# Optimization experiments

Hardware: AMD Instinct MI355X
Metric: run time of the kernel (lower is better)

## Reference

```python
import jax, jax.numpy as jnp
from jax import lax
import numpy as np

B, S, D, H, O, V = 1024, 128, 256, 2048, 10, 10

def setup_inputs() -> dict:
    key = jax.random.key(0)
    ks = jax.random.split(key, 8)
    x = jax.random.randint(ks[0], (B, S), 0, V)
    embed = jax.random.normal(ks[1], (V, D), dtype=jnp.float32)
    sd_hx = 1.0 / np.sqrt(D)
    sd_hh = 1.0 / np.sqrt(H)
    W_hx = jax.random.uniform(ks[2], (H, D), minval=-sd_hx, maxval=sd_hx)
    b_hx = jax.random.uniform(ks[3], (H,), minval=-sd_hx, maxval=sd_hx)
    W_hh = jax.random.uniform(ks[4], (H, H), minval=-sd_hh, maxval=sd_hh)
    b_hh = jax.random.uniform(ks[5], (H,), minval=-sd_hh, maxval=sd_hh)
    W_oh = jax.random.uniform(ks[6], (O, H), minval=-sd_hh, maxval=sd_hh)
    b_oh = jax.random.uniform(ks[7], (O,), minval=-sd_hh, maxval=sd_hh)
    return {"x": x, "embed": embed, "W_hx": W_hx, "b_hx": b_hx,
            "W_hh": W_hh, "b_hh": b_hh, "W_oh": W_oh, "b_oh": b_oh}

def reference(x, embed, W_hx, b_hx, W_hh, b_hh, W_oh, b_oh):
    e = embed[x]                                   # [B,S,D]
    # precompute input-to-hidden projection for all steps (one big GEMM)
    xh = jnp.einsum('bsd,hd->bsh', e, W_hx) + b_hx  # [B,S,H]
    # step 0: torch code applies ONLY hx (no hh term, no hh bias)
    h0 = jnp.tanh(xh[:, 0])
    def step(h, xt):
        h = jnp.tanh(xt + h @ W_hh.T + b_hh)
        return h, None
    hT, _ = lax.scan(step, h0, jnp.swapaxes(xh[:, 1:], 0, 1))  # scan over time
    o = hT @ W_oh.T + b_oh                         # [B,O]
    return jax.nn.softmax(o, axis=1)               # nn.Softmax() on 2D -> dim=1
```

## Files before the change

kernel.cpp:

```cpp
#include <hip/hip_runtime.h>
#include <stdint.h>
#include <stddef.h>

#define B_ 1024
#define S_ 128
#define D_ 256
#define H_ 2048
#define O_ 10
#define V_ 10

#define BM 128
#define BN 64
#define BK 128
#define NKT (H_ / BK)
#define NSTG 3
#define STG_ELEMS ((BM + BN) * BK)
#define SMEM_BYTES (NSTG * STG_ELEMS * 2)

typedef unsigned short u16;
typedef short v8s __attribute__((ext_vector_type(8)));
typedef float v4f __attribute__((ext_vector_type(4)));
typedef u16 u16x4 __attribute__((ext_vector_type(4)));

__device__ __forceinline__ u16 f2bf(float f) {
  unsigned int u = __float_as_uint(f);
  u += 0x7FFFu + ((u >> 16) & 1u);
  return (u16)(u >> 16);
}
__device__ __forceinline__ float bf2f(u16 h) {
  return __uint_as_float(((unsigned int)h) << 16);
}
__device__ __forceinline__ float fast_tanh(float x) {
  float e = __expf(2.0f * x);
  return 1.0f - 2.0f / (e + 1.0f);
}
__device__ __forceinline__ void gl2lds16(const void* g, void* l) {
  __builtin_amdgcn_global_load_lds(
      (const __attribute__((address_space(1))) uint32_t*)g,
      (__attribute__((address_space(3))) uint32_t*)l, 16, 0, 0);
}

__global__ __launch_bounds__(256) void make_table(const float* __restrict__ embed,
                                                  const float* __restrict__ W_hx,
                                                  const float* __restrict__ b_hx,
                                                  float* __restrict__ Txh) {
  int idx = blockIdx.x * 256 + threadIdx.x;
  int v = idx >> 11, h = idx & 2047;
  const float4* e4 = (const float4*)(embed + v * D_);
  const float4* w4 = (const float4*)(W_hx + (size_t)h * D_);
  float s = b_hx[h];
#pragma unroll 4
  for (int d = 0; d < D_ / 4; ++d) {
    float4 a = e4[d], b = w4[d];
    s = fmaf(a.x, b.x, s); s = fmaf(a.y, b.y, s);
    s = fmaf(a.z, b.z, s); s = fmaf(a.w, b.w, s);
  }
  Txh[idx] = s;
}

__global__ __launch_bounds__(256) void conv_w(const float* __restrict__ W,
                                              u16* __restrict__ Wb) {
  int i = blockIdx.x * 256 + threadIdx.x;
  float4 w = ((const float4*)W)[i];
  u16x4 o = { f2bf(w.x), f2bf(w.y), f2bf(w.z), f2bf(w.w) };
  ((u16x4*)Wb)[i] = o;
}

__global__ __launch_bounds__(256) void init_h0(const float* __restrict__ Txh,
                                               const int* __restrict__ x,
                                               u16* __restrict__ H0) {
  int idx = blockIdx.x * 256 + threadIdx.x;
  int b = idx >> 11, j = idx & 2047;
  int xv = x[b * S_];
  H0[idx] = f2bf(fast_tanh(Txh[xv * H_ + j]));
}


__global__ __launch_bounds__(256, 1) void rnn_step(const u16* __restrict__ Hin,
                                                   const u16* __restrict__ Wb,
                                                   const float* __restrict__ Txh,
                                                   const int* __restrict__ x,
                                                   const float* __restrict__ b_hh,
                                                   u16* __restrict__ Hout,
                                                   int t) {
  extern __shared__ __align__(16) u16 smem[];

  const int tid = threadIdx.x;
  const int bid = blockIdx.x;
  const int xcd = bid & 7;
  const int sl  = bid >> 3;
  const int xr = xcd >> 2, xc = xcd & 3;
  const int bm = (xr * 4 + (sl >> 3)) * BM;
  const int bn = (xc * 8 + (sl & 7)) * BN;

  const int w = tid >> 6, l = tid & 63;
  const int wr = w >> 1, wc = w & 1;
  const int lane16 = l & 15, quad = l >> 4;
  const int wbase = w << 6;

  unsigned offA[8], offB[4];
#pragma unroll
  for (int i = 0; i < 8; ++i) {
    int s = i * 256 + tid;
    int m = s >> 4;
    int cg = (s & 15) ^ (m & 15);
    offA[i] = (unsigned)((bm + m) * H_ + cg * 8);
  }
#pragma unroll
  for (int i = 0; i < 4; ++i) {
    int s = i * 256 + tid;
    int n = s >> 4;
    int cg = (s & 15) ^ (n & 15);
    offB[i] = (unsigned)((bn + n) * H_ + cg * 8);
  }

#define STAGE(stg, kbase) do {                                              \
    u16* As_ = smem + (stg) * STG_ELEMS;                                    \
    u16* Bs_ = As_ + BM * BK;                                               \
    _Pragma("unroll")                                                       \
    for (int i_ = 0; i_ < 8; ++i_)                                          \
      gl2lds16(Hin + offA[i_] + (kbase), As_ + (size_t)(i_ * 256 + wbase) * 8); \
    _Pragma("unroll")                                                       \
    for (int i_ = 0; i_ < 4; ++i_)                                          \
      gl2lds16(Wb + offB[i_] + (kbase), Bs_ + (size_t)(i_ * 256 + wbase) * 8);  \
  } while (0)

  v4f acc[4][2];
#pragma unroll
  for (int i = 0; i < 4; ++i)
#pragma unroll
    for (int j = 0; j < 2; ++j) acc[i][j] = (v4f){0.f, 0.f, 0.f, 0.f};

  STAGE(0, 0);
  STAGE(1, BK);

  for (int kt = 0; kt < NKT; ++kt) {
    __builtin_amdgcn_s_barrier();
    asm volatile("" ::: "memory");

    if (kt + 2 < NKT) STAGE((kt + 2) % 3, (kt + 2) * BK);

    if (kt < NKT - 2)       asm volatile("s_waitcnt vmcnt(24)" ::: "memory");
    else if (kt == NKT - 2) asm volatile("s_waitcnt vmcnt(12)" ::: "memory");
    else                    asm volatile("s_waitcnt vmcnt(0)"  ::: "memory");

    __builtin_amdgcn_s_barrier();
    asm volatile("" ::: "memory");

    const u16* Asb = smem + (kt % 3) * STG_ELEMS;
    const u16* Bsb = Asb + BM * BK;

    v8s aX[4], bX[2], aY[4], bY[2];
#define LDSET(AV, BV, kc) do {                                              \
    const int cc_ = (kc) * 4 + quad;                                        \
    _Pragma("unroll")                                                       \
    for (int i_ = 0; i_ < 4; ++i_) {                                        \
      int m_ = wr * 64 + i_ * 16 + lane16;     \
      AV[i_] = *(const v8s*)&Asb[(size_t)(m_ * 16 + (cc_ ^ lane16)) * 8];   \
    }                                                                       \
    _Pragma("unroll")                                                       \
    for (int j_ = 0; j_ < 2; ++j_) {                                        \
      int n_ = wc * 32 + j_ * 16 + lane16;                                  \
      BV[j_] = *(const v8s*)&Bsb[(size_t)(n_ * 16 + (cc_ ^ lane16)) * 8];   \
    }                                                                       \
  } while (0)
#define MM(AV, BV) do {                                                     \
    _Pragma("unroll")                                                       \
    for (int i_ = 0; i_ < 4; ++i_)                                          \
      _Pragma("unroll")                                                     \
      for (int j_ = 0; j_ < 2; ++j_)                                        \
        acc[i_][j_] = __builtin_amdgcn_mfma_f32_16x16x32_bf16(              \
            AV[i_], BV[j_], acc[i_][j_], 0, 0, 0);                          \
  } while (0)

    LDSET(aX, bX, 0);
    LDSET(aY, bY, 1);
    __builtin_amdgcn_s_setprio(1);
    MM(aX, bX);
    LDSET(aX, bX, 2);
    MM(aY, bY);
    LDSET(aY, bY, 3);
    MM(aX, bX);
    MM(aY, bY);
    __builtin_amdgcn_s_setprio(0);
#undef LDSET
#undef MM
  }
#undef STAGE

  float bh[2];
#pragma unroll
  for (int j = 0; j < 2; ++j) bh[j] = b_hh[bn + wc * 32 + j * 16 + lane16];
#pragma unroll
  for (int i = 0; i < 4; ++i) {
#pragma unroll
    for (int r = 0; r < 4; ++r) {
      int row = bm + wr * 64 + i * 16 + quad * 4 + r;
      const float* trow = Txh + x[row * S_ + t] * H_;
      u16* orow = Hout + (size_t)row * H_;
#pragma unroll
      for (int j = 0; j < 2; ++j) {
        int col = bn + wc * 32 + j * 16 + lane16;
        float v = acc[i][j][r] + trow[col] + bh[j];
        orow[col] = f2bf(fast_tanh(v));
      }
    }
  }
}

__global__ __launch_bounds__(256) void out_softmax(const u16* __restrict__ Hf,
                                                   const float* __restrict__ W_oh,
                                                   const float* __restrict__ b_oh,
                                                   float* __restrict__ out) {
  int b = blockIdx.x, tid = threadIdx.x;
  float hv[8];
  const u16* hr = Hf + (size_t)b * H_ + tid * 8;
#pragma unroll
  for (int u = 0; u < 8; ++u) hv[u] = bf2f(hr[u]);
  float acc[O_];
#pragma unroll
  for (int i = 0; i < O_; ++i) {
    const float* wr = W_oh + (size_t)i * H_ + tid * 8;
    float s = 0.f;
#pragma unroll
    for (int u = 0; u < 8; ++u) s = fmaf(hv[u], wr[u], s);
    acc[i] = s;
  }
#pragma unroll
  for (int off = 32; off > 0; off >>= 1)
#pragma unroll
    for (int i = 0; i < O_; ++i) acc[i] += __shfl_down(acc[i], off);
  __shared__ float red[4][O_];
  if ((tid & 63) == 0)
#pragma unroll
    for (int i = 0; i < O_; ++i) red[tid >> 6][i] = acc[i];
  __syncthreads();
  if (tid == 0) {
    float o[O_], mx = -1e30f;
#pragma unroll
    for (int i = 0; i < O_; ++i) {
      o[i] = red[0][i] + red[1][i] + red[2][i] + red[3][i] + b_oh[i];
      mx = fmaxf(mx, o[i]);
    }
    float se = 0.f;
#pragma unroll
    for (int i = 0; i < O_; ++i) { o[i] = __expf(o[i] - mx); se += o[i]; }
    float inv = 1.f / se;
#pragma unroll
    for (int i = 0; i < O_; ++i) out[b * O_ + i] = o[i] * inv;
  }
}

extern "C" void kernel_launch(void* const* d_in, const int* in_sizes, int n_in,
                              void* d_out, int out_size, void* d_ws, size_t ws_size,
                              hipStream_t stream) {
  const int*   x     = (const int*)  d_in[0];
  const float* embed = (const float*)d_in[1];
  const float* W_hx  = (const float*)d_in[2];
  const float* b_hx  = (const float*)d_in[3];
  const float* W_hh  = (const float*)d_in[4];
  const float* b_hh  = (const float*)d_in[5];
  const float* W_oh  = (const float*)d_in[6];
  const float* b_oh  = (const float*)d_in[7];
  float* out = (float*)d_out;

  static bool attr_set = false;
  if (!attr_set) {
    (void)hipFuncSetAttribute(reinterpret_cast<const void*>(rnn_step),
                              hipFuncAttributeMaxDynamicSharedMemorySize, SMEM_BYTES);
    attr_set = true;
  }

  char* ws = (char*)d_ws;
  float* Txh = (float*)ws;
  u16* Wb = (u16*)(ws + (80 << 10));
  u16* Ha = (u16*)(ws + (80 << 10) + (8 << 20));
  u16* Hb = (u16*)(ws + (80 << 10) + (12 << 20));

  make_table<<<80, 256, 0, stream>>>(embed, W_hx, b_hx, Txh);
  conv_w<<<4096, 256, 0, stream>>>(W_hh, Wb);
  init_h0<<<8192, 256, 0, stream>>>(Txh, x, Ha);

  for (int t = 1; t < S_; ++t) {
    const u16* hin = (t & 1) ? Ha : Hb;
    u16* hout = (t & 1) ? Hb : Ha;
    rnn_step<<<256, 256, SMEM_BYTES, stream>>>(hin, Wb, Txh, x, b_hh, hout, t);
  }
  out_softmax<<<B_, 256, 0, stream>>>(Hb, W_oh, b_oh, out);
}
```

Before: 2.354 ms.

## Fuse RNN time steps into persistent cooperative kernel with per-group barriers

Replaces the 127 per-step kernel launches with a single cooperative persistent kernel that loops over time. Each group of 32 workgroups shares one 128-row batch slice, so they sync through per-group atomic counters instead of a grid-wide barrier. This removes launch overhead and lets different batch groups drift apart in time, at the cost of spin-wait latency and losing the XCD-aware tile mapping. It also adds an lgkmcnt wait before the stage barrier, and keeps the old per-step launches as a fallback.

```diff
diff --git a/kernel.cpp b/kernel.cpp
--- a/kernel.cpp
+++ b/kernel.cpp
@@ -16,6 +16,8 @@
 #define NSTG 3
 #define STG_ELEMS ((BM + BN) * BK)
 #define SMEM_BYTES (NSTG * STG_ELEMS * 2)
+#define NGRP 8
+#define GRP_WGS 32
 
 typedef unsigned short u16;
 typedef short v8s __attribute__((ext_vector_type(8)));
@@ -76,6 +78,155 @@
 }
 
 
+__global__ __launch_bounds__(256, 1) void rnn_persist(const u16* __restrict__ Wb,
+                                                      const float* __restrict__ Txh,
+                                                      const int* __restrict__ x,
+                                                      const float* __restrict__ b_hh,
+                                                      u16* __restrict__ Ha,
+                                                      u16* __restrict__ Hb,
+                                                      unsigned int* __restrict__ cnt) {
+  extern __shared__ __align__(16) u16 smem[];
+
+  const int tid = threadIdx.x;
+  const int bid = blockIdx.x;
+  const int g = bid >> 5;
+  const int bm = g * BM;
+  const int bn = (bid & 31) * BN;
+
+  const int w = tid >> 6, l = tid & 63;
+  const int wr = w >> 1, wc = w & 1;
+  const int lane16 = l & 15, quad = l >> 4;
+  const int wbase = w << 6;
+
+  unsigned offA[8], offB[4];
+#pragma unroll
+  for (int i = 0; i < 8; ++i) {
+    int s = i * 256 + tid;
+    int m = s >> 4;
+    int cg = (s & 15) ^ (m & 15);
+    offA[i] = (unsigned)((bm + m) * H_ + cg * 8);
+  }
+#pragma unroll
+  for (int i = 0; i < 4; ++i) {
+    int s = i * 256 + tid;
+    int n = s >> 4;
+    int cg = (s & 15) ^ (n & 15);
+    offB[i] = (unsigned)((bn + n) * H_ + cg * 8);
+  }
+
+#define STAGE(stg, kbase, HINP) do {                                        \
+    u16* As_ = smem + (stg) * STG_ELEMS;                                    \
+    u16* Bs_ = As_ + BM * BK;                                               \
+    _Pragma("unroll")                                                       \
+    for (int i_ = 0; i_ < 8; ++i_)                                          \
+      gl2lds16((HINP) + offA[i_] + (kbase), As_ + (size_t)(i_ * 256 + wbase) * 8); \
+    _Pragma("unroll")                                                       \
+    for (int i_ = 0; i_ < 4; ++i_)                                          \
+      gl2lds16(Wb + offB[i_] + (kbase), Bs_ + (size_t)(i_ * 256 + wbase) * 8);  \
+  } while (0)
+
+  float bh[2];
+#pragma unroll
+  for (int j = 0; j < 2; ++j) bh[j] = b_hh[bn + wc * 32 + j * 16 + lane16];
+
+  for (int t = 1; t < S_; ++t) {
+    const u16* Hin = (t & 1) ? Ha : Hb;
+    u16* Hout = (t & 1) ? Hb : Ha;
+
+    STAGE(0, 0, Hin);
+    STAGE(1, BK, Hin);
+
+    v4f acc[4][2];
+#pragma unroll
+    for (int i = 0; i < 4; ++i)
+#pragma unroll
+      for (int j = 0; j < 2; ++j) acc[i][j] = (v4f){0.f, 0.f, 0.f, 0.f};
+
+    for (int kt = 0; kt < NKT; ++kt) {
+      asm volatile("s_waitcnt lgkmcnt(0)" ::: "memory");
+      __builtin_amdgcn_s_barrier();
+      asm volatile("" ::: "memory");
+
+      if (kt + 2 < NKT) STAGE((kt + 2) % 3, (kt + 2) * BK, Hin);
+
+      if (kt < NKT - 2)       asm volatile("s_waitcnt vmcnt(24)" ::: "memory");
+      else if (kt == NKT - 2) asm volatile("s_waitcnt vmcnt(12)" ::: "memory");
+      else                    asm volatile("s_waitcnt vmcnt(0)"  ::: "memory");
+
+      __builtin_amdgcn_s_barrier();
+      asm volatile("" ::: "memory");
+
+      const u16* Asb = smem + (kt % 3) * STG_ELEMS;
+      const u16* Bsb = Asb + BM * BK;
+
+      v8s aX[4], bX[2], aY[4], bY[2];
+#define LDSET(AV, BV, kc) do {                                              \
+    const int cc_ = (kc) * 4 + quad;                                        \
+    _Pragma("unroll")                                                       \
+    for (int i_ = 0; i_ < 4; ++i_) {                                        \
+      int m_ = wr * 64 + i_ * 16 + lane16;     \
+      AV[i_] = *(const v8s*)&Asb[(size_t)(m_ * 16 + (cc_ ^ lane16)) * 8];   \
+    }                                                                       \
+    _Pragma("unroll")                                                       \
+    for (int j_ = 0; j_ < 2; ++j_) {                                        \
+      int n_ = wc * 32 + j_ * 16 + lane16;                                  \
+      BV[j_] = *(const v8s*)&Bsb[(size_t)(n_ * 16 + (cc_ ^ lane16)) * 8];   \
+    }                                                                       \
+  } while (0)
+#define MM(AV, BV) do {                                                     \
+    _Pragma("unroll")                                                       \
+    for (int i_ = 0; i_ < 4; ++i_)                                          \
+      _Pragma("unroll")                                                     \
+      for (int j_ = 0; j_ < 2; ++j_)                                        \
+        acc[i_][j_] = __builtin_amdgcn_mfma_f32_16x16x32_bf16(              \
+            AV[i_], BV[j_], acc[i_][j_], 0, 0, 0);                          \
+  } while (0)
+
+      LDSET(aX, bX, 0);
+      LDSET(aY, bY, 1);
+      __builtin_amdgcn_s_setprio(1);
+      MM(aX, bX);
+      LDSET(aX, bX, 2);
+      MM(aY, bY);
+      LDSET(aY, bY, 3);
+      MM(aX, bX);
+      MM(aY, bY);
+      __builtin_amdgcn_s_setprio(0);
+#undef LDSET
+#undef MM
+    }
+
+#pragma unroll
+    for (int i = 0; i < 4; ++i) {
+#pragma unroll
+      for (int r = 0; r < 4; ++r) {
+        int row = bm + wr * 64 + i * 16 + quad * 4 + r;
+        const float* trow = Txh + x[row * S_ + t] * H_;
+        u16* orow = Hout + (size_t)row * H_;
+#pragma unroll
+        for (int j = 0; j < 2; ++j) {
+          int col = bn + wc * 32 + j * 16 + lane16;
+          float v = acc[i][j][r] + trow[col] + bh[j];
+          orow[col] = f2bf(fast_tanh(v));
+        }
+      }
+    }
+
+    if (t + 1 < S_) {
+      __syncthreads();
+      if (tid == 0) {
+        unsigned int* c = cnt + g * S_ + t;
+        __hip_atomic_fetch_add(c, 1u, __ATOMIC_RELEASE, __HIP_MEMORY_SCOPE_AGENT);
+        while (__hip_atomic_load(c, __ATOMIC_RELAXED, __HIP_MEMORY_SCOPE_AGENT) < GRP_WGS)
+          __builtin_amdgcn_s_sleep(2);
+        (void)__hip_atomic_fetch_add(c, 0u, __ATOMIC_ACQ_REL, __HIP_MEMORY_SCOPE_AGENT);
+      }
+      __syncthreads();
+    }
+  }
+#undef STAGE
+}
+
 __global__ __launch_bounds__(256, 1) void rnn_step(const u16* __restrict__ Hin,
                                                    const u16* __restrict__ Wb,
                                                    const float* __restrict__ Txh,
@@ -114,7 +265,7 @@
     offB[i] = (unsigned)((bn + n) * H_ + cg * 8);
   }
 
-#define STAGE(stg, kbase) do {                                              \
+#define STAGE1(stg, kbase) do {                                             \
     u16* As_ = smem + (stg) * STG_ELEMS;                                    \
     u16* Bs_ = As_ + BM * BK;                                               \
     _Pragma("unroll")                                                       \
@@ -131,14 +282,15 @@
 #pragma unroll
     for (int j = 0; j < 2; ++j) acc[i][j] = (v4f){0.f, 0.f, 0.f, 0.f};
 
-  STAGE(0, 0);
-  STAGE(1, BK);
+  STAGE1(0, 0);
+  STAGE1(1, BK);
 
   for (int kt = 0; kt < NKT; ++kt) {
+    asm volatile("s_waitcnt lgkmcnt(0)" ::: "memory");
     __builtin_amdgcn_s_barrier();
     asm volatile("" ::: "memory");
 
-    if (kt + 2 < NKT) STAGE((kt + 2) % 3, (kt + 2) * BK);
+    if (kt + 2 < NKT) STAGE1((kt + 2) % 3, (kt + 2) * BK);
 
     if (kt < NKT - 2)       asm volatile("s_waitcnt vmcnt(24)" ::: "memory");
     else if (kt == NKT - 2) asm volatile("s_waitcnt vmcnt(12)" ::: "memory");
@@ -155,7 +307,7 @@
     const int cc_ = (kc) * 4 + quad;                                        \
     _Pragma("unroll")                                                       \
     for (int i_ = 0; i_ < 4; ++i_) {                                        \
-      int m_ = wr * 64 + i_ * 16 + lane16;     \
+      int m_ = wr * 64 + i_ * 16 + lane16;                                  \
       AV[i_] = *(const v8s*)&Asb[(size_t)(m_ * 16 + (cc_ ^ lane16)) * 8];   \
     }                                                                       \
     _Pragma("unroll")                                                       \
@@ -186,7 +338,7 @@
 #undef LDSET
 #undef MM
   }
-#undef STAGE
+#undef STAGE1
 
   float bh[2];
 #pragma unroll
@@ -266,6 +418,8 @@
 
   static bool attr_set = false;
   if (!attr_set) {
+    (void)hipFuncSetAttribute(reinterpret_cast<const void*>(rnn_persist),
+                              hipFuncAttributeMaxDynamicSharedMemorySize, SMEM_BYTES);
     (void)hipFuncSetAttribute(reinterpret_cast<const void*>(rnn_step),
                               hipFuncAttributeMaxDynamicSharedMemorySize, SMEM_BYTES);
     attr_set = true;
@@ -276,15 +430,25 @@
   u16* Wb = (u16*)(ws + (80 << 10));
   u16* Ha = (u16*)(ws + (80 << 10) + (8 << 20));
   u16* Hb = (u16*)(ws + (80 << 10) + (12 << 20));
-
+  unsigned int* cnt = (unsigned int*)(ws + (80 << 10) + (16 << 20));
+
+  hipMemsetAsync(cnt, 0, NGRP * S_ * sizeof(unsigned int), stream);
   make_table<<<80, 256, 0, stream>>>(embed, W_hx, b_hx, Txh);
   conv_w<<<4096, 256, 0, stream>>>(W_hh, Wb);
   init_h0<<<8192, 256, 0, stream>>>(Txh, x, Ha);
 
-  for (int t = 1; t < S_; ++t) {
-    const u16* hin = (t & 1) ? Ha : Hb;
-    u16* hout = (t & 1) ? Hb : Ha;
-    rnn_step<<<256, 256, SMEM_BYTES, stream>>>(hin, Wb, Txh, x, b_hh, hout, t);
+  const u16* Wb_c = Wb;  const float* Txh_c = Txh;
+  void* args[] = { (void*)&Wb_c, (void*)&Txh_c, (void*)&x, (void*)&b_hh,
+                   (void*)&Ha, (void*)&Hb, (void*)&cnt };
+  hipError_t ce = hipLaunchCooperativeKernel((const void*)rnn_persist,
+                                             dim3(256), dim3(256),
+                                             args, SMEM_BYTES, stream);
+  if (ce != hipSuccess) {
+    for (int t = 1; t < S_; ++t) {
+      const u16* hin = (t & 1) ? Ha : Hb;
+      u16* hout = (t & 1) ? Hb : Ha;
+      rnn_step<<<256, 256, SMEM_BYTES, stream>>>(hin, Wb, Txh, x, b_hh, hout, t);
+    }
   }
   out_softmax<<<B_, 256, 0, stream>>>(Hb, W_oh, b_oh, out);
 }
```

Measured after the change: 3.714 ms. +57.8%, slower.

## Load hidden-state operand directly from global into registers, stage only weights in LDS

Applied to the files above, without the earlier changes.

The A operand (previous hidden state) is no longer staged through shared memory. Each wave now loads its own A fragments straight into registers with inline global_load_dwordx4, and the MFMA chunks are ordered behind staggered vmcnt waits. Only the W_hh tile stays triple-buffered in static LDS, which shrinks shared memory and removes the A LDS write/read round trip. The cost is that A rows are fetched twice, once by each column wave, and global load latency sits right before use with no multi-stage prefetch, so the kernel relies on L2 hits and the partial waits to hide it.

```diff
diff --git a/kernel.cpp b/kernel.cpp
--- a/kernel.cpp
+++ b/kernel.cpp
@@ -14,8 +14,7 @@
 #define BK 128
 #define NKT (H_ / BK)
 #define NSTG 3
-#define STG_ELEMS ((BM + BN) * BK)
-#define SMEM_BYTES (NSTG * STG_ELEMS * 2)
+#define BSTG (BN * BK)
 
 typedef unsigned short u16;
 typedef short v8s __attribute__((ext_vector_type(8)));
@@ -76,6 +75,9 @@
 }
 
 
+#define WAITV(N) asm volatile("s_waitcnt vmcnt(" #N ")" ::: "memory")
+#define SB0 __builtin_amdgcn_sched_barrier(0)
+
 __global__ __launch_bounds__(256, 1) void rnn_step(const u16* __restrict__ Hin,
                                                    const u16* __restrict__ Wb,
                                                    const float* __restrict__ Txh,
@@ -83,7 +85,7 @@
                                                    const float* __restrict__ b_hh,
                                                    u16* __restrict__ Hout,
                                                    int t) {
-  extern __shared__ __align__(16) u16 smem[];
+  __shared__ __align__(16) u16 Bst[NSTG][BSTG];
 
   const int tid = threadIdx.x;
   const int bid = blockIdx.x;
@@ -98,14 +100,7 @@
   const int lane16 = l & 15, quad = l >> 4;
   const int wbase = w << 6;
 
-  unsigned offA[8], offB[4];
-#pragma unroll
-  for (int i = 0; i < 8; ++i) {
-    int s = i * 256 + tid;
-    int m = s >> 4;
-    int cg = (s & 15) ^ (m & 15);
-    offA[i] = (unsigned)((bm + m) * H_ + cg * 8);
-  }
+  unsigned offB[4];
 #pragma unroll
   for (int i = 0; i < 4; ++i) {
     int s = i * 256 + tid;
@@ -113,57 +108,36 @@
     int cg = (s & 15) ^ (n & 15);
     offB[i] = (unsigned)((bn + n) * H_ + cg * 8);
   }
-
-#define STAGE(stg, kbase) do {                                              \
-    u16* As_ = smem + (stg) * STG_ELEMS;                                    \
-    u16* Bs_ = As_ + BM * BK;                                               \
-    _Pragma("unroll")                                                       \
-    for (int i_ = 0; i_ < 8; ++i_)                                          \
-      gl2lds16(Hin + offA[i_] + (kbase), As_ + (size_t)(i_ * 256 + wbase) * 8); \
+  unsigned voffA[4];
+#pragma unroll
+  for (int i = 0; i < 4; ++i)
+    voffA[i] = (unsigned)(((bm + wr * 64 + i * 16 + lane16) * H_ + quad * 8) * 2);
+
+#define STAGE_W(stg, kbase) do {                                            \
+    u16* Bs_ = &Bst[stg][0];                                                \
     _Pragma("unroll")                                                       \
     for (int i_ = 0; i_ < 4; ++i_)                                          \
-      gl2lds16(Wb + offB[i_] + (kbase), Bs_ + (size_t)(i_ * 256 + wbase) * 8);  \
-  } while (0)
-
-  v4f acc[4][2];
-#pragma unroll
-  for (int i = 0; i < 4; ++i)
-#pragma unroll
-    for (int j = 0; j < 2; ++j) acc[i][j] = (v4f){0.f, 0.f, 0.f, 0.f};
-
-  STAGE(0, 0);
-  STAGE(1, BK);
-
-  for (int kt = 0; kt < NKT; ++kt) {
-    __builtin_amdgcn_s_barrier();
-    asm volatile("" ::: "memory");
-
-    if (kt + 2 < NKT) STAGE((kt + 2) % 3, (kt + 2) * BK);
-
-    if (kt < NKT - 2)       asm volatile("s_waitcnt vmcnt(24)" ::: "memory");
-    else if (kt == NKT - 2) asm volatile("s_waitcnt vmcnt(12)" ::: "memory");
-    else                    asm volatile("s_waitcnt vmcnt(0)"  ::: "memory");
-
-    __builtin_amdgcn_s_barrier();
-    asm volatile("" ::: "memory");
-
-    const u16* Asb = smem + (kt % 3) * STG_ELEMS;
-    const u16* Bsb = Asb + BM * BK;
-
-    v8s aX[4], bX[2], aY[4], bY[2];
-#define LDSET(AV, BV, kc) do {                                              \
-    const int cc_ = (kc) * 4 + quad;                                        \
-    _Pragma("unroll")                                                       \
-    for (int i_ = 0; i_ < 4; ++i_) {                                        \
-      int m_ = wr * 64 + i_ * 16 + lane16;     \
-      AV[i_] = *(const v8s*)&Asb[(size_t)(m_ * 16 + (cc_ ^ lane16)) * 8];   \
-    }                                                                       \
+      gl2lds16(Wb + offB[i_] + (kbase), Bs_ + (size_t)(i_ * 256 + wbase) * 8); \
+  } while (0)
+
+#define ALD(SET, VK, OFFLIT) do {                                           \
+    _Pragma("unroll")                                                       \
+    for (int i_ = 0; i_ < 4; ++i_)                                          \
+      asm volatile("global_load_dwordx4 %0, %1, %2 offset:%3"               \
+                   : "=v"(SET[i_])                                          \
+                   : "v"(VK[i_]), "s"(Hin), "n"(OFFLIT)                     \
+                   : "memory");                                             \
+  } while (0)
+
+#define BSET(BV, KC) do {                                                   \
+    const int cc_ = (KC) * 4 + quad;                                        \
     _Pragma("unroll")                                                       \
     for (int j_ = 0; j_ < 2; ++j_) {                                        \
       int n_ = wc * 32 + j_ * 16 + lane16;                                  \
       BV[j_] = *(const v8s*)&Bsb[(size_t)(n_ * 16 + (cc_ ^ lane16)) * 8];   \
     }                                                                       \
   } while (0)
+
 #define MM(AV, BV) do {                                                     \
     _Pragma("unroll")                                                       \
     for (int i_ = 0; i_ < 4; ++i_)                                          \
@@ -173,20 +147,60 @@
             AV[i_], BV[j_], acc[i_][j_], 0, 0, 0);                          \
   } while (0)
 
-    LDSET(aX, bX, 0);
-    LDSET(aY, bY, 1);
-    __builtin_amdgcn_s_setprio(1);
-    MM(aX, bX);
-    LDSET(aX, bX, 2);
-    MM(aY, bY);
-    LDSET(aY, bY, 3);
-    MM(aX, bX);
-    MM(aY, bY);
-    __builtin_amdgcn_s_setprio(0);
-#undef LDSET
+  v4f acc[4][2];
+#pragma unroll
+  for (int i = 0; i < 4; ++i)
+#pragma unroll
+    for (int j = 0; j < 2; ++j) acc[i][j] = (v4f){0.f, 0.f, 0.f, 0.f};
+
+  STAGE_W(0, 0);
+  STAGE_W(1, BK);
+  WAITV(4);
+  __builtin_amdgcn_s_barrier();
+  asm volatile("" ::: "memory");
+
+  int cur = 0, pre = 2;
+  for (int kt = 0; kt < NKT; ++kt) {
+    asm volatile("s_waitcnt lgkmcnt(0)" ::: "memory");
+    __builtin_amdgcn_s_barrier();
+    asm volatile("" ::: "memory");
+
+    unsigned vk[4];
+#pragma unroll
+    for (int i = 0; i < 4; ++i) vk[i] = voffA[i] + (unsigned)(kt * 256);
+    v8s a0[4], a1[4], a2[4], a3[4];
+    ALD(a0, vk, 0);
+    ALD(a1, vk, 64);
+    ALD(a2, vk, 128);
+    ALD(a3, vk, 192);
+    if (kt + 2 < NKT) STAGE_W(pre, (kt + 2) * BK);
+
+    const u16* Bsb = &Bst[cur][0];
+    v8s bX[2], bY[2];
+    BSET(bX, 0);
+    BSET(bY, 1);
+    if (kt < NKT - 2) { WAITV(16); } else { WAITV(12); }
+    SB0;
+    MM(a0, bX);
+    BSET(bX, 2);
+    if (kt < NKT - 2) { WAITV(12); } else { WAITV(8); }
+    SB0;
+    MM(a1, bY);
+    BSET(bY, 3);
+    if (kt < NKT - 2) { WAITV(8); } else { WAITV(4); }
+    SB0;
+    MM(a2, bX);
+    if (kt < NKT - 2) { WAITV(4); } else { WAITV(0); }
+    SB0;
+    MM(a3, bY);
+
+    cur = (cur == 2) ? 0 : cur + 1;
+    pre = (pre == 2) ? 0 : pre + 1;
+  }
+#undef STAGE_W
+#undef ALD
+#undef BSET
 #undef MM
-  }
-#undef STAGE
 
   float bh[2];
 #pragma unroll
@@ -264,13 +278,6 @@
   const float* b_oh  = (const float*)d_in[7];
   float* out = (float*)d_out;
 
-  static bool attr_set = false;
-  if (!attr_set) {
-    (void)hipFuncSetAttribute(reinterpret_cast<const void*>(rnn_step),
-                              hipFuncAttributeMaxDynamicSharedMemorySize, SMEM_BYTES);
-    attr_set = true;
-  }
-
   char* ws = (char*)d_ws;
   float* Txh = (float*)ws;
   u16* Wb = (u16*)(ws + (80 << 10));
@@ -284,7 +291,7 @@
   for (int t = 1; t < S_; ++t) {
     const u16* hin = (t & 1) ? Ha : Hb;
     u16* hout = (t & 1) ? Hb : Ha;
-    rnn_step<<<256, 256, SMEM_BYTES, stream>>>(hin, Wb, Txh, x, b_hh, hout, t);
+    rnn_step<<<256, 256, 0, stream>>>(hin, Wb, Txh, x, b_hh, hout, t);
   }
   out_softmax<<<B_, 256, 0, stream>>>(Hb, W_oh, b_oh, out);
 }
```

New measurement: 4.981 ms. 2.12x slower.
